# Kernel tuning notes

Hardware: AMD Instinct MI355X
Metric: run time of the kernel (lower is better)

## Reference

```python
import jax, jax.numpy as jnp
import numpy as np

B, N, DIM, HEADS, DIM_HEAD = 2, 2048, 1024, 16, 64
INNER = HEADS * DIM_HEAD  # 1024
SCALE = DIM_HEAD ** -0.5
EPS = 1e-5  # fp32 path in the source


def _layernorm_seq(x, g):
    # Faithful to the repo's LayerNorm: statistics over dim=1 (sequence axis),
    # unbiased=False variance, clamp(min=eps).rsqrt(), scale by g over last axis.
    mean = jnp.mean(x, axis=1, keepdims=True)            # [b,1,d]
    var = jnp.mean((x - mean) ** 2, axis=1, keepdims=True)
    return (x - mean) * jax.lax.rsqrt(jnp.maximum(var, EPS)) * g


def setup_inputs() -> dict:
    key = jax.random.key(0)
    ks = jax.random.split(key, 5)
    x = jax.random.normal(ks[0], (B, N, DIM), dtype=jnp.float32)
    rel_pos_bias = jax.random.normal(ks[1], (1, HEADS, N, N), dtype=jnp.float32)
    g = jnp.ones((DIM,), dtype=jnp.float32)
    wq = jax.random.normal(ks[2], (INNER, DIM), dtype=jnp.float32) * (DIM ** -0.5)
    wkv = jax.random.normal(ks[3], (2 * INNER, DIM), dtype=jnp.float32) * (DIM ** -0.5)
    wout = jax.random.normal(ks[4], (DIM, INNER), dtype=jnp.float32) * (INNER ** -0.5)
    return {"x": x, "rel_pos_bias": rel_pos_bias, "g": g, "wq": wq, "wkv": wkv, "wout": wout}


def reference(x, rel_pos_bias, g, wq, wkv, wout):
    # self-attention path: context = x, framerate = None
    xn = _layernorm_seq(x, g)           # [b,n,d]
    cn = xn                              # context is None -> same tensor, same norm
    q = jnp.einsum('bnd,ed->bne', xn, wq)        # [b,n,inner]
    kv = jnp.einsum('bnd,ed->bne', cn, wkv)      # [b,n,2*inner]
    k, v = jnp.split(kv, 2, axis=-1)
    def heads(t):
        return t.reshape(B, N, HEADS, DIM_HEAD).transpose(0, 2, 1, 3)  # b h n d
    q, k, v = heads(q) * SCALE, heads(k), heads(v)
    sim = jnp.einsum('bhid,bhjd->bhij', q, k) + rel_pos_bias
    attn = jax.nn.softmax(sim, axis=-1)
    out = jnp.einsum('bhij,bhjd->bhid', attn, v)
    out = out.transpose(0, 2, 1, 3).reshape(B, N, INNER)  # b n (h d)
    return jnp.einsum('bne,de->bnd', out, wout)
```

## Files before the change

kernel.cpp:

```cpp
#include <hip/hip_runtime.h>
#include <hip/hip_bf16.h>
#include <stdint.h>

#define B_ 2
#define N_ 2048
#define DIM_ 1024
#define HEADS_ 16
#define DH_ 64
#define EPS_ 1e-5f

typedef __attribute__((ext_vector_type(4))) float f32x4;
typedef __attribute__((ext_vector_type(8))) __bf16 bf16x8;
typedef __attribute__((ext_vector_type(4))) unsigned int u32x4;

__device__ __forceinline__ f32x4 mfma16(bf16x8 a, bf16x8 b, f32x4 c) {
  return __builtin_amdgcn_mfma_f32_16x16x32_bf16(a, b, c, 0, 0, 0);
}

__device__ __forceinline__ unsigned short f2bf(float x) {
  unsigned int u = __builtin_bit_cast(unsigned int, x);
  u += 0x7fffu + ((u >> 16) & 1u);
  return (unsigned short)(u >> 16);
}

__device__ __forceinline__ unsigned int cvt_pk_bf16(float lo, float hi) {
  unsigned int r;
  asm("v_cvt_pk_bf16_f32 %0, %1, %2" : "=v"(r) : "v"(lo), "v"(hi));
  return r;
}

__device__ __forceinline__ bf16x8 ld_frag(const unsigned short* p) {
  u32x4 v = *reinterpret_cast<const u32x4*>(p);
  return __builtin_bit_cast(bf16x8, v);
}

__device__ __forceinline__ void gload_lds16(const unsigned short* g, unsigned short* l) {
  __builtin_amdgcn_global_load_lds((const __attribute__((address_space(1))) void*)g,
                                   (__attribute__((address_space(3))) void*)l, 16, 0, 0);
}

__global__ __launch_bounds__(256) void ln_part(const float* __restrict__ x,
                                               float* __restrict__ ps,
                                               float* __restrict__ pss) {
  const int d = blockIdx.x * 256 + threadIdx.x;
  const int b = blockIdx.y >> 4, sp = blockIdx.y & 15;
  const float* xp = x + (size_t)(b * N_ + sp * 128) * DIM_ + d;
  float s = 0.f, ss = 0.f;
  for (int i = 0; i < 128; ++i) {
    float v = xp[(size_t)i * DIM_];
    s += v;
    ss += v * v;
  }
  int c = b * DIM_ + d;
  ps[sp * (B_ * DIM_) + c] = s;
  pss[sp * (B_ * DIM_) + c] = ss;
}

__global__ void ln_fin(const float* __restrict__ ps, const float* __restrict__ pss,
                       const float* __restrict__ g, float* __restrict__ meanA,
                       float* __restrict__ sclA) {
  int c = blockIdx.x * 256 + threadIdx.x;
  float s = 0.f, ss = 0.f;
#pragma unroll
  for (int sp = 0; sp < 16; ++sp) {
    s += ps[sp * (B_ * DIM_) + c];
    ss += pss[sp * (B_ * DIM_) + c];
  }
  float m = s * (1.f / N_);
  float v = ss * (1.f / N_) - m * m;
  meanA[c] = m;
  sclA[c] = rsqrtf(fmaxf(v, EPS_)) * g[c & (DIM_ - 1)];
}

__global__ __launch_bounds__(256) void ln_apply(const float* __restrict__ x,
                                                const float* __restrict__ meanA,
                                                const float* __restrict__ sclA,
                                                unsigned short* __restrict__ xn) {
  size_t t = (size_t)blockIdx.x * 256 + threadIdx.x;
  size_t base = t * 8;
  int d0 = (int)(base & (DIM_ - 1));
  int b = base >= (size_t)N_ * DIM_;
  int c = b * DIM_ + d0;
  const float4* xp = reinterpret_cast<const float4*>(x + base);
  const float4* mp = reinterpret_cast<const float4*>(meanA + c);
  const float4* sp = reinterpret_cast<const float4*>(sclA + c);
  float4 x0 = xp[0], x1 = xp[1];
  float4 m0 = mp[0], m1 = mp[1];
  float4 s0 = sp[0], s1 = sp[1];
  union {
    unsigned short u[8];
    u32x4 v;
  } o;
  o.u[0] = f2bf((x0.x - m0.x) * s0.x);
  o.u[1] = f2bf((x0.y - m0.y) * s0.y);
  o.u[2] = f2bf((x0.z - m0.z) * s0.z);
  o.u[3] = f2bf((x0.w - m0.w) * s0.w);
  o.u[4] = f2bf((x1.x - m1.x) * s1.x);
  o.u[5] = f2bf((x1.y - m1.y) * s1.y);
  o.u[6] = f2bf((x1.z - m1.z) * s1.z);
  o.u[7] = f2bf((x1.w - m1.w) * s1.w);
  *reinterpret_cast<u32x4*>(xn + base) = o.v;
}

__global__ __launch_bounds__(256) void cast_bf16(const float* __restrict__ src,
                                                 unsigned short* __restrict__ dst, float scale) {
  size_t t = (size_t)blockIdx.x * 256 + threadIdx.x;
  size_t base = t * 8;
  const float4* sp = reinterpret_cast<const float4*>(src + base);
  float4 a = sp[0], b4 = sp[1];
  union {
    unsigned short u[8];
    u32x4 v;
  } o;
  o.u[0] = f2bf(a.x * scale);
  o.u[1] = f2bf(a.y * scale);
  o.u[2] = f2bf(a.z * scale);
  o.u[3] = f2bf(a.w * scale);
  o.u[4] = f2bf(b4.x * scale);
  o.u[5] = f2bf(b4.y * scale);
  o.u[6] = f2bf(b4.z * scale);
  o.u[7] = f2bf(b4.w * scale);
  *reinterpret_cast<u32x4*>(dst + base) = o.v;
}

template <bool OUT_F32>
__global__ __launch_bounds__(256) void gemm_bt(const unsigned short* __restrict__ A,
                                               const unsigned short* __restrict__ W,
                                               void* __restrict__ Cout, int K, int ldc) {
  __shared__ unsigned short sA[128 * 64];
  __shared__ unsigned short sB[128 * 64];
  const int tid = threadIdx.x, lane = tid & 63, w = tid >> 6;
  const int wm = w >> 1, wn = w & 1;
  const int l15 = lane & 15, l4 = lane >> 4;
  const int m0 = blockIdx.y * 128, n0 = blockIdx.x * 128;
  f32x4 acc[4][4] = {};
  for (int kt = 0; kt < K; kt += 64) {
    __syncthreads();
#pragma unroll
    for (int p = 0; p < 4; ++p) {
      int flat = p * 256 + tid;
      int row = flat >> 3, c = flat & 7;
      int cs = c ^ (row & 7);
      gload_lds16(A + (size_t)(m0 + row) * K + kt + cs * 8, sA + (size_t)(p * 256 + w * 64) * 8);
      gload_lds16(W + (size_t)(n0 + row) * K + kt + cs * 8, sB + (size_t)(p * 256 + w * 64) * 8);
    }
    __syncthreads();
#pragma unroll
    for (int kk = 0; kk < 2; ++kk) {
      bf16x8 af[4], bfr[4];
#pragma unroll
      for (int i = 0; i < 4; ++i) {
        int rowA = wm * 64 + i * 16 + l15;
        af[i] = ld_frag(sA + rowA * 64 + (((kk * 4 + l4) ^ (rowA & 7)) * 8));
        int rowB = wn * 64 + i * 16 + l15;
        bfr[i] = ld_frag(sB + rowB * 64 + (((kk * 4 + l4) ^ (rowB & 7)) * 8));
      }
#pragma unroll
      for (int i = 0; i < 4; ++i)
#pragma unroll
        for (int j = 0; j < 4; ++j) acc[i][j] = mfma16(af[i], bfr[j], acc[i][j]);
    }
  }
#pragma unroll
  for (int i = 0; i < 4; ++i)
#pragma unroll
    for (int j = 0; j < 4; ++j)
#pragma unroll
      for (int r = 0; r < 4; ++r) {
        size_t off =
            (size_t)(m0 + wm * 64 + i * 16 + l4 * 4 + r) * ldc + (n0 + wn * 64 + j * 16 + l15);
        if (OUT_F32)
          ((float*)Cout)[off] = acc[i][j][r];
        else
          ((unsigned short*)Cout)[off] = f2bf(acc[i][j][r]);
      }
}

__global__ __launch_bounds__(256) void transpose_v(const unsigned short* __restrict__ qkv,
                                                   unsigned short* __restrict__ Vt) {
  __shared__ unsigned short tt[64][65];
  const int tid = threadIdx.x;
  const int h = blockIdx.y >> 1, b = blockIdx.y & 1;
  const int n0 = blockIdx.x * 64;
  const unsigned short* src = qkv + (size_t)(b * N_ + n0) * 3072 + 2048 + h * 64;
#pragma unroll
  for (int i = 0; i < 16; ++i) {
    int idx = i * 256 + tid;
    int r = idx >> 6, c = idx & 63;
    tt[r][c] = src[(size_t)r * 3072 + c];
  }
  __syncthreads();
  unsigned short* dst = Vt + (size_t)(b * HEADS_ + h) * 64 * N_ + n0;
#pragma unroll
  for (int i = 0; i < 16; ++i) {
    int idx = i * 256 + tid;
    int dh = idx >> 6, nn = idx & 63;
    dst[(size_t)dh * N_ + nn] = tt[nn][dh];
  }
}

__global__ __launch_bounds__(512, 4) void flash_attn(const unsigned short* __restrict__ qkv,
                                                     const float* __restrict__ bias,
                                                     const unsigned short* __restrict__ Vt,
                                                     unsigned short* __restrict__ Oatt) {
  __shared__ unsigned short sK[2][64 * 64];
  __shared__ unsigned short sV[2][64 * 64];
  __shared__ unsigned short sP[8 * 16 * 64];

  const int tid = threadIdx.x, lane = tid & 63, w = tid >> 6;
  const int l15 = lane & 15, l4 = lane >> 4;
  const int r = blockIdx.x;
  const int bh = r & 31, iblk = r >> 5;
  const int h = bh & 15, b = bh >> 4;
  const int i0 = iblk * 128;

  const unsigned short* Kg = qkv + (size_t)b * N_ * 3072 + 1024 + h * 64;
  const unsigned short* VtB = Vt + (size_t)(b * HEADS_ + h) * 64 * N_;
  const float* bias_q =
      bias + (size_t)h * N_ * N_ + (size_t)(i0 + w * 16 + l15) * N_ + l4 * 4;

  const int srow = tid >> 3, sc = tid & 7;
  const int scs = sc ^ (srow & 7);
  const size_t kSrcOff = (size_t)srow * 3072 + (size_t)scs * 8;
  const size_t vSrcOff = (size_t)srow * N_ + (size_t)scs * 8;
  unsigned short* kDst0 = sK[0] + (size_t)w * 512;
  unsigned short* kDst1 = sK[1] + (size_t)w * 512;
  unsigned short* vDst0 = sV[0] + (size_t)w * 512;
  unsigned short* vDst1 = sV[1] + (size_t)w * 512;

  bf16x8 qf[2];
  {
    const unsigned short* Qg =
        qkv + (size_t)(b * N_ + i0 + w * 16 + l15) * 3072 + h * 64 + l4 * 8;
    qf[0] = ld_frag(Qg);
    qf[1] = ld_frag(Qg + 32);
  }

  f32x4 o_t[4] = {};
  f32x4 stA[4], stB[4];
  float m_run = -1e30f, l_run = 0.f;
  const int sw = l15 & 7;

  unsigned int* sPu = reinterpret_cast<unsigned int*>(sP + (size_t)w * 16 * 64);
  const unsigned short* sPw = sP + (size_t)w * 16 * 64;

  gload_lds16(Kg + kSrcOff, kDst0);
  gload_lds16(VtB + vSrcOff, vDst0);
  stA[0] = *reinterpret_cast<const f32x4*>(bias_q);
  stA[1] = *reinterpret_cast<const f32x4*>(bias_q + 16);
  stA[2] = *reinterpret_cast<const f32x4*>(bias_q + 32);
  stA[3] = *reinterpret_cast<const f32x4*>(bias_q + 48);
  __syncthreads();

  const int NT = N_ / 64;

#define TILE_BODY(T, SKC, SVC, KDN, VDN, SC, SN)                               \
  {                                                                            \
    if ((T) + 1 < NT) {                                                        \
      const size_t jn = (size_t)((T) + 1) * 64;                                \
      gload_lds16(Kg + jn * 3072 + kSrcOff, KDN);                              \
      gload_lds16(VtB + jn + vSrcOff, VDN);                                    \
      __builtin_amdgcn_sched_barrier(0);  \
      SN[0] = *reinterpret_cast<const f32x4*>(bias_q + jn);                    \
      SN[1] = *reinterpret_cast<const f32x4*>(bias_q + jn + 16);               \
      SN[2] = *reinterpret_cast<const f32x4*>(bias_q + jn + 32);               \
      SN[3] = *reinterpret_cast<const f32x4*>(bias_q + jn + 48);               \
    }                                                                          \
                 \
    __builtin_amdgcn_s_setprio(1);                                             \
    _Pragma("unroll") for (int kj = 0; kj < 4; ++kj) {                         \
      int row = kj * 16 + l15;                                                 \
      bf16x8 kf0 = ld_frag(SKC + row * 64 + ((l4 ^ sw) * 8));                  \
      bf16x8 kf1 = ld_frag(SKC + row * 64 + (((4 + l4) ^ sw) * 8));            \
      SC[kj] = mfma16(kf0, qf[0], SC[kj]);                                     \
      SC[kj] = mfma16(kf1, qf[1], SC[kj]);                                     \
    }                                                                          \
    __builtin_amdgcn_s_setprio(0);                                             \
                  \
    float mx = fmaxf(fmaxf(fmaxf(SC[0][0], SC[0][1]), fmaxf(SC[0][2], SC[0][3])), \
                     fmaxf(fmaxf(SC[1][0], SC[1][1]), fmaxf(SC[1][2], SC[1][3]))); \
    mx = fmaxf(mx, fmaxf(fmaxf(fmaxf(SC[2][0], SC[2][1]), fmaxf(SC[2][2], SC[2][3])), \
                         fmaxf(fmaxf(SC[3][0], SC[3][1]), fmaxf(SC[3][2], SC[3][3])))); \
    mx = fmaxf(mx, __shfl_xor(mx, 16));                                        \
    mx = fmaxf(mx, __shfl_xor(mx, 32));                                        \
    float mn = fmaxf(m_run, mx);                                               \
    float alpha = __expf(m_run - mn);                                          \
    float rs = 0.f;                                                            \
    _Pragma("unroll") for (int kj = 0; kj < 4; ++kj) {                         \
      _Pragma("unroll") for (int rr = 0; rr < 4; ++rr) {                       \
        float p = __expf(SC[kj][rr] - mn);                                     \
        SC[kj][rr] = p;                                                        \
        rs += p;                                                               \
      }                                                                        \
    }                                                                          \
    rs += __shfl_xor(rs, 16);                                                  \
    rs += __shfl_xor(rs, 32);                                                  \
    l_run = l_run * alpha + rs;                                                \
    m_run = mn;                                                                \
    _Pragma("unroll") for (int dj = 0; dj < 4; ++dj) {                         \
      o_t[dj][0] *= alpha;                                                     \
      o_t[dj][1] *= alpha;                                                     \
      o_t[dj][2] *= alpha;                                                     \
      o_t[dj][3] *= alpha;                                                     \
    }                                                                          \
         \
    _Pragma("unroll") for (int kj = 0; kj < 4; ++kj) {                         \
      unsigned int v0 = cvt_pk_bf16(SC[kj][0], SC[kj][1]);                     \
      unsigned int v1 = cvt_pk_bf16(SC[kj][2], SC[kj][3]);                     \
      int cc = (kj * 2 + (l4 >> 1)) ^ sw;                                      \
      uint2 pv;                                                                \
      pv.x = v0;                                                               \
      pv.y = v1;                                                               \
      *reinterpret_cast<uint2*>(sPu + l15 * 32 + cc * 4 + (l4 & 1) * 2) = pv;  \
    }                                                                          \
                                                           \
    bf16x8 pb0 = ld_frag(sPw + l15 * 64 + ((l4 ^ sw) * 8));                    \
    bf16x8 pb1 = ld_frag(sPw + l15 * 64 + (((4 + l4) ^ sw) * 8));              \
    __builtin_amdgcn_s_setprio(1);                                             \
    _Pragma("unroll") for (int dj = 0; dj < 4; ++dj) {                         \
      int row = dj * 16 + l15;                                                 \
      bf16x8 vf0 = ld_frag(SVC + row * 64 + ((l4 ^ sw) * 8));                  \
      bf16x8 vf1 = ld_frag(SVC + row * 64 + (((4 + l4) ^ sw) * 8));            \
      o_t[dj] = mfma16(vf0, pb0, o_t[dj]);                                     \
      o_t[dj] = mfma16(vf1, pb1, o_t[dj]);                                     \
    }                                                                          \
    __builtin_amdgcn_s_setprio(0);                                             \
    if ((T) != NT - 1) {                                                       \
          \
                    \
      asm volatile("s_waitcnt vmcnt(4)" ::: "memory");                         \
      __builtin_amdgcn_s_barrier();                                            \
    }                                                                          \
  }

  const unsigned short* sK0c = sK[0];
  const unsigned short* sK1c = sK[1];
  const unsigned short* sV0c = sV[0];
  const unsigned short* sV1c = sV[1];
  for (int t = 0; t < NT; t += 2) {
    TILE_BODY(t, sK0c, sV0c, kDst1, vDst1, stA, stB)
    TILE_BODY(t + 1, sK1c, sV1c, kDst0, vDst0, stB, stA)
  }
#undef TILE_BODY

  float inv = 1.f / l_run;
  unsigned short* orow =
      Oatt + (size_t)(b * N_ + i0 + w * 16 + l15) * 1024 + h * 64 + l4 * 4;
#pragma unroll
  for (int dj = 0; dj < 4; ++dj) {
    union {
      unsigned short u[4];
      unsigned long long v;
    } pk;
    pk.u[0] = f2bf(o_t[dj][0] * inv);
    pk.u[1] = f2bf(o_t[dj][1] * inv);
    pk.u[2] = f2bf(o_t[dj][2] * inv);
    pk.u[3] = f2bf(o_t[dj][3] * inv);
    *reinterpret_cast<unsigned long long*>(orow + dj * 16) = pk.v;
  }
}

extern "C" void kernel_launch(void* const* d_in, const int* in_sizes, int n_in, void* d_out,
                              int out_size, void* d_ws, size_t ws_size, hipStream_t stream) {
  const float* x = (const float*)d_in[0];
  const float* bias = (const float*)d_in[1];
  const float* g = (const float*)d_in[2];
  const float* wq = (const float*)d_in[3];
  const float* wkv = (const float*)d_in[4];
  const float* wout = (const float*)d_in[5];
  float* out = (float*)d_out;

  float* ps = (float*)d_ws;
  float* pss = ps + 16 * B_ * DIM_;
  float* meanA = pss + 16 * B_ * DIM_;
  float* sclA = meanA + B_ * DIM_;
  unsigned short* xn = (unsigned short*)(sclA + B_ * DIM_);
  unsigned short* Wqkv = xn + (size_t)4096 * 1024;
  unsigned short* WoutB = Wqkv + (size_t)3072 * 1024;
  unsigned short* qkvb = WoutB + (size_t)1024 * 1024;
  unsigned short* Vt = qkvb + (size_t)4096 * 3072;
  unsigned short* Oatt = xn;

  ln_part<<<dim3(DIM_ / 256, B_ * 16), 256, 0, stream>>>(x, ps, pss);
  ln_fin<<<dim3((B_ * DIM_) / 256), 256, 0, stream>>>(ps, pss, g, meanA, sclA);
  ln_apply<<<dim3((B_ * N_ * DIM_) / 2048), 256, 0, stream>>>(x, meanA, sclA, xn);
  cast_bf16<<<dim3((DIM_ * DIM_) / 2048), 256, 0, stream>>>(wq, Wqkv, 0.125f);
  cast_bf16<<<dim3((2 * DIM_ * DIM_) / 2048), 256, 0, stream>>>(wkv, Wqkv + (size_t)DIM_ * DIM_,
                                                                1.0f);
  cast_bf16<<<dim3((DIM_ * DIM_) / 2048), 256, 0, stream>>>(wout, WoutB, 1.0f);
  gemm_bt<false><<<dim3(3072 / 128, 4096 / 128), 256, 0, stream>>>(xn, Wqkv, qkvb, DIM_, 3072);
  transpose_v<<<dim3(N_ / 64, B_ * HEADS_), 256, 0, stream>>>(qkvb, Vt);
  flash_attn<<<dim3(512), 512, 0, stream>>>(qkvb, bias, Vt, Oatt);
  gemm_bt<true><<<dim3(1024 / 128, 4096 / 128), 256, 0, stream>>>(Oatt, WoutB, out, DIM_, 1024);
}
```

Before: 190.2 us.

## Give each attention wave 32 query rows to reuse K/V fragments across two tiles

The flash attention kernel now runs 4 waves of 256 threads per block instead of 8. Each wave handles two 16-row query fragments and reuses every K and V fragment it loads from LDS for both. Staging is split into four async loads per thread, the vmcnt wait is raised to match, and softmax state is duplicated per fragment. This halves LDS fragment reads per MFMA but doubles accumulator and bias registers per thread, which lowers occupancy and leaves fewer waves to hide the latency of the fp32 bias loads.

```diff
diff --git a/kernel.cpp b/kernel.cpp
--- a/kernel.cpp
+++ b/kernel.cpp
@@ -199,13 +199,13 @@
   }
 }
 
-__global__ __launch_bounds__(512, 4) void flash_attn(const unsigned short* __restrict__ qkv,
+__global__ __launch_bounds__(256, 2) void flash_attn(const unsigned short* __restrict__ qkv,
                                                      const float* __restrict__ bias,
                                                      const unsigned short* __restrict__ Vt,
                                                      unsigned short* __restrict__ Oatt) {
   __shared__ unsigned short sK[2][64 * 64];
   __shared__ unsigned short sV[2][64 * 64];
-  __shared__ unsigned short sP[8 * 16 * 64];
+  __shared__ unsigned short sP[4 * 32 * 64];
 
   const int tid = threadIdx.x, lane = tid & 63, w = tid >> 6;
   const int l15 = lane & 15, l4 = lane >> 4;
@@ -213,150 +213,199 @@
   const int bh = r & 31, iblk = r >> 5;
   const int h = bh & 15, b = bh >> 4;
   const int i0 = iblk * 128;
+  const int qbase = i0 + w * 32;
 
   const unsigned short* Kg = qkv + (size_t)b * N_ * 3072 + 1024 + h * 64;
   const unsigned short* VtB = Vt + (size_t)(b * HEADS_ + h) * 64 * N_;
-  const float* bias_q =
-      bias + (size_t)h * N_ * N_ + (size_t)(i0 + w * 16 + l15) * N_ + l4 * 4;
-
-  const int srow = tid >> 3, sc = tid & 7;
-  const int scs = sc ^ (srow & 7);
-  const size_t kSrcOff = (size_t)srow * 3072 + (size_t)scs * 8;
-  const size_t vSrcOff = (size_t)srow * N_ + (size_t)scs * 8;
-  unsigned short* kDst0 = sK[0] + (size_t)w * 512;
-  unsigned short* kDst1 = sK[1] + (size_t)w * 512;
-  unsigned short* vDst0 = sV[0] + (size_t)w * 512;
-  unsigned short* vDst1 = sV[1] + (size_t)w * 512;
-
-  bf16x8 qf[2];
+  const float* bias_q0 =
+      bias + (size_t)h * N_ * N_ + (size_t)(qbase + l15) * N_ + l4 * 4;
+  const float* bias_q1 = bias_q0 + 16 * N_;
+
+  const int row0 = tid >> 3, c0 = tid & 7;
+  const int cs0 = c0 ^ (row0 & 7);
+  const unsigned short* KgS = Kg + (size_t)row0 * 3072 + cs0 * 8;
+  const unsigned short* VtS = VtB + (size_t)row0 * N_ + cs0 * 8;
+
+#define STAGE(BUF, JN)                                                     \
+  gload_lds16(KgS + (size_t)(JN) * 3072, sK[BUF] + w * 512);               \
+  gload_lds16(KgS + (size_t)(JN) * 3072 + 32 * 3072, sK[BUF] + 2048 + w * 512); \
+  gload_lds16(VtS + (JN), sV[BUF] + w * 512);                              \
+  gload_lds16(VtS + (JN) + 32 * (size_t)N_, sV[BUF] + 2048 + w * 512);
+
+  bf16x8 qf00, qf01, qf10, qf11;
   {
-    const unsigned short* Qg =
-        qkv + (size_t)(b * N_ + i0 + w * 16 + l15) * 3072 + h * 64 + l4 * 8;
-    qf[0] = ld_frag(Qg);
-    qf[1] = ld_frag(Qg + 32);
-  }
-
-  f32x4 o_t[4] = {};
-  f32x4 stA[4], stB[4];
-  float m_run = -1e30f, l_run = 0.f;
+    const unsigned short* Qg0 =
+        qkv + (size_t)(b * N_ + qbase + l15) * 3072 + h * 64 + l4 * 8;
+    const unsigned short* Qg1 = Qg0 + (size_t)16 * 3072;
+    qf00 = ld_frag(Qg0);
+    qf01 = ld_frag(Qg0 + 32);
+    qf10 = ld_frag(Qg1);
+    qf11 = ld_frag(Qg1 + 32);
+  }
+
+  f32x4 o_t[8] = {};
+  f32x4 stA[8], stB[8];
+  float m0_run = -1e30f, l0_run = 0.f;
+  float m1_run = -1e30f, l1_run = 0.f;
   const int sw = l15 & 7;
 
-  unsigned int* sPu = reinterpret_cast<unsigned int*>(sP + (size_t)w * 16 * 64);
-  const unsigned short* sPw = sP + (size_t)w * 16 * 64;
-
-  gload_lds16(Kg + kSrcOff, kDst0);
-  gload_lds16(VtB + vSrcOff, vDst0);
-  stA[0] = *reinterpret_cast<const f32x4*>(bias_q);
-  stA[1] = *reinterpret_cast<const f32x4*>(bias_q + 16);
-  stA[2] = *reinterpret_cast<const f32x4*>(bias_q + 32);
-  stA[3] = *reinterpret_cast<const f32x4*>(bias_q + 48);
+  unsigned int* sPu = reinterpret_cast<unsigned int*>(sP + (size_t)w * 2048);
+  const unsigned short* sPw = sP + (size_t)w * 2048;
+
+  STAGE(0, 0)
+#pragma unroll
+  for (int kj = 0; kj < 4; ++kj) {
+    stA[kj] = *reinterpret_cast<const f32x4*>(bias_q0 + kj * 16);
+    stA[4 + kj] = *reinterpret_cast<const f32x4*>(bias_q1 + kj * 16);
+  }
   __syncthreads();
 
   const int NT = N_ / 64;
 
-#define TILE_BODY(T, SKC, SVC, KDN, VDN, SC, SN)                               \
+#define TILE_BODY(T, CUR, NXT, SC, SN)                                         \
   {                                                                            \
     if ((T) + 1 < NT) {                                                        \
       const size_t jn = (size_t)((T) + 1) * 64;                                \
-      gload_lds16(Kg + jn * 3072 + kSrcOff, KDN);                              \
-      gload_lds16(VtB + jn + vSrcOff, VDN);                                    \
+      STAGE(NXT, jn)                                                           \
       __builtin_amdgcn_sched_barrier(0);  \
-      SN[0] = *reinterpret_cast<const f32x4*>(bias_q + jn);                    \
-      SN[1] = *reinterpret_cast<const f32x4*>(bias_q + jn + 16);               \
-      SN[2] = *reinterpret_cast<const f32x4*>(bias_q + jn + 32);               \
-      SN[3] = *reinterpret_cast<const f32x4*>(bias_q + jn + 48);               \
-    }                                                                          \
-                 \
+      _Pragma("unroll") for (int kj = 0; kj < 4; ++kj) {                       \
+        SN[kj] = *reinterpret_cast<const f32x4*>(bias_q0 + jn + kj * 16);      \
+        SN[4 + kj] = *reinterpret_cast<const f32x4*>(bias_q1 + jn + kj * 16);  \
+      }                                                                        \
+    }                                                                          \
+    const unsigned short* sKc = sK[CUR];                                       \
+    const unsigned short* sVc = sV[CUR];                                       \
+                  \
     __builtin_amdgcn_s_setprio(1);                                             \
     _Pragma("unroll") for (int kj = 0; kj < 4; ++kj) {                         \
       int row = kj * 16 + l15;                                                 \
-      bf16x8 kf0 = ld_frag(SKC + row * 64 + ((l4 ^ sw) * 8));                  \
-      bf16x8 kf1 = ld_frag(SKC + row * 64 + (((4 + l4) ^ sw) * 8));            \
-      SC[kj] = mfma16(kf0, qf[0], SC[kj]);                                     \
-      SC[kj] = mfma16(kf1, qf[1], SC[kj]);                                     \
+      bf16x8 kf0 = ld_frag(sKc + row * 64 + ((l4 ^ sw) * 8));                  \
+      bf16x8 kf1 = ld_frag(sKc + row * 64 + (((4 + l4) ^ sw) * 8));            \
+      SC[kj] = mfma16(kf0, qf00, SC[kj]);                                      \
+      SC[kj] = mfma16(kf1, qf01, SC[kj]);                                      \
+      SC[4 + kj] = mfma16(kf0, qf10, SC[4 + kj]);                              \
+      SC[4 + kj] = mfma16(kf1, qf11, SC[4 + kj]);                              \
     }                                                                          \
     __builtin_amdgcn_s_setprio(0);                                             \
-                  \
-    float mx = fmaxf(fmaxf(fmaxf(SC[0][0], SC[0][1]), fmaxf(SC[0][2], SC[0][3])), \
-                     fmaxf(fmaxf(SC[1][0], SC[1][1]), fmaxf(SC[1][2], SC[1][3]))); \
-    mx = fmaxf(mx, fmaxf(fmaxf(fmaxf(SC[2][0], SC[2][1]), fmaxf(SC[2][2], SC[2][3])), \
-                         fmaxf(fmaxf(SC[3][0], SC[3][1]), fmaxf(SC[3][2], SC[3][3])))); \
-    mx = fmaxf(mx, __shfl_xor(mx, 16));                                        \
-    mx = fmaxf(mx, __shfl_xor(mx, 32));                                        \
-    float mn = fmaxf(m_run, mx);                                               \
-    float alpha = __expf(m_run - mn);                                          \
-    float rs = 0.f;                                                            \
-    _Pragma("unroll") for (int kj = 0; kj < 4; ++kj) {                         \
-      _Pragma("unroll") for (int rr = 0; rr < 4; ++rr) {                       \
-        float p = __expf(SC[kj][rr] - mn);                                     \
-        SC[kj][rr] = p;                                                        \
-        rs += p;                                                               \
-      }                                                                        \
-    }                                                                          \
-    rs += __shfl_xor(rs, 16);                                                  \
-    rs += __shfl_xor(rs, 32);                                                  \
-    l_run = l_run * alpha + rs;                                                \
-    m_run = mn;                                                                \
-    _Pragma("unroll") for (int dj = 0; dj < 4; ++dj) {                         \
-      o_t[dj][0] *= alpha;                                                     \
-      o_t[dj][1] *= alpha;                                                     \
-      o_t[dj][2] *= alpha;                                                     \
-      o_t[dj][3] *= alpha;                                                     \
-    }                                                                          \
-         \
-    _Pragma("unroll") for (int kj = 0; kj < 4; ++kj) {                         \
-      unsigned int v0 = cvt_pk_bf16(SC[kj][0], SC[kj][1]);                     \
-      unsigned int v1 = cvt_pk_bf16(SC[kj][2], SC[kj][3]);                     \
-      int cc = (kj * 2 + (l4 >> 1)) ^ sw;                                      \
-      uint2 pv;                                                                \
-      pv.x = v0;                                                               \
-      pv.y = v1;                                                               \
-      *reinterpret_cast<uint2*>(sPu + l15 * 32 + cc * 4 + (l4 & 1) * 2) = pv;  \
-    }                                                                          \
-                                                           \
-    bf16x8 pb0 = ld_frag(sPw + l15 * 64 + ((l4 ^ sw) * 8));                    \
-    bf16x8 pb1 = ld_frag(sPw + l15 * 64 + (((4 + l4) ^ sw) * 8));              \
+                               \
+    {                                                                          \
+      float mx = fmaxf(fmaxf(fmaxf(SC[0][0], SC[0][1]), fmaxf(SC[0][2], SC[0][3])), \
+                       fmaxf(fmaxf(SC[1][0], SC[1][1]), fmaxf(SC[1][2], SC[1][3]))); \
+      mx = fmaxf(mx, fmaxf(fmaxf(fmaxf(SC[2][0], SC[2][1]), fmaxf(SC[2][2], SC[2][3])), \
+                           fmaxf(fmaxf(SC[3][0], SC[3][1]), fmaxf(SC[3][2], SC[3][3])))); \
+      mx = fmaxf(mx, __shfl_xor(mx, 16));                                      \
+      mx = fmaxf(mx, __shfl_xor(mx, 32));                                      \
+      float mn = fmaxf(m0_run, mx);                                            \
+      float alpha = __expf(m0_run - mn);                                       \
+      float rs = 0.f;                                                          \
+      _Pragma("unroll") for (int kj = 0; kj < 4; ++kj) {                       \
+        _Pragma("unroll") for (int rr = 0; rr < 4; ++rr) {                     \
+          float p = __expf(SC[kj][rr] - mn);                                   \
+          SC[kj][rr] = p;                                                      \
+          rs += p;                                                             \
+        }                                                                      \
+      }                                                                        \
+      rs += __shfl_xor(rs, 16);                                                \
+      rs += __shfl_xor(rs, 32);                                                \
+      l0_run = l0_run * alpha + rs;                                            \
+      m0_run = mn;                                                             \
+      _Pragma("unroll") for (int dj = 0; dj < 4; ++dj) {                       \
+        o_t[dj][0] *= alpha;                                                   \
+        o_t[dj][1] *= alpha;                                                   \
+        o_t[dj][2] *= alpha;                                                   \
+        o_t[dj][3] *= alpha;                                                   \
+      }                                                                        \
+    }                                                                          \
+                          \
+    {                                                                          \
+      float mx = fmaxf(fmaxf(fmaxf(SC[4][0], SC[4][1]), fmaxf(SC[4][2], SC[4][3])), \
+                       fmaxf(fmaxf(SC[5][0], SC[5][1]), fmaxf(SC[5][2], SC[5][3]))); \
+      mx = fmaxf(mx, fmaxf(fmaxf(fmaxf(SC[6][0], SC[6][1]), fmaxf(SC[6][2], SC[6][3])), \
+                           fmaxf(fmaxf(SC[7][0], SC[7][1]), fmaxf(SC[7][2], SC[7][3])))); \
+      mx = fmaxf(mx, __shfl_xor(mx, 16));                                      \
+      mx = fmaxf(mx, __shfl_xor(mx, 32));                                      \
+      float mn = fmaxf(m1_run, mx);                                            \
+      float alpha = __expf(m1_run - mn);                                       \
+      float rs = 0.f;                                                          \
+      _Pragma("unroll") for (int kj = 0; kj < 4; ++kj) {                       \
+        _Pragma("unroll") for (int rr = 0; rr < 4; ++rr) {                     \
+          float p = __expf(SC[4 + kj][rr] - mn);                               \
+          SC[4 + kj][rr] = p;                                                  \
+          rs += p;                                                             \
+        }                                                                      \
+      }                                                                        \
+      rs += __shfl_xor(rs, 16);                                                \
+      rs += __shfl_xor(rs, 32);                                                \
+      l1_run = l1_run * alpha + rs;                                            \
+      m1_run = mn;                                                             \
+      _Pragma("unroll") for (int dj = 0; dj < 4; ++dj) {                       \
+        o_t[4 + dj][0] *= alpha;                                               \
+        o_t[4 + dj][1] *= alpha;                                               \
+        o_t[4 + dj][2] *= alpha;                                               \
+        o_t[4 + dj][3] *= alpha;                                               \
+      }                                                                        \
+    }                                                                          \
+                   \
+    _Pragma("unroll") for (int f = 0; f < 2; ++f) {                            \
+      _Pragma("unroll") for (int kj = 0; kj < 4; ++kj) {                       \
+        unsigned int v0 = cvt_pk_bf16(SC[f * 4 + kj][0], SC[f * 4 + kj][1]);   \
+        unsigned int v1 = cvt_pk_bf16(SC[f * 4 + kj][2], SC[f * 4 + kj][3]);   \
+        int cc = (kj * 2 + (l4 >> 1)) ^ sw;                                    \
+        uint2 pv;                                                              \
+        pv.x = v0;                                                             \
+        pv.y = v1;                                                             \
+        *reinterpret_cast<uint2*>(sPu + (f * 16 + l15) * 32 + cc * 4 +         \
+                                  (l4 & 1) * 2) = pv;                          \
+      }                                                                        \
+    }                                                                          \
+                                 \
+    bf16x8 pb00 = ld_frag(sPw + l15 * 64 + ((l4 ^ sw) * 8));                   \
+    bf16x8 pb01 = ld_frag(sPw + l15 * 64 + (((4 + l4) ^ sw) * 8));             \
+    bf16x8 pb10 = ld_frag(sPw + (16 + l15) * 64 + ((l4 ^ sw) * 8));            \
+    bf16x8 pb11 = ld_frag(sPw + (16 + l15) * 64 + (((4 + l4) ^ sw) * 8));      \
     __builtin_amdgcn_s_setprio(1);                                             \
     _Pragma("unroll") for (int dj = 0; dj < 4; ++dj) {                         \
       int row = dj * 16 + l15;                                                 \
-      bf16x8 vf0 = ld_frag(SVC + row * 64 + ((l4 ^ sw) * 8));                  \
-      bf16x8 vf1 = ld_frag(SVC + row * 64 + (((4 + l4) ^ sw) * 8));            \
-      o_t[dj] = mfma16(vf0, pb0, o_t[dj]);                                     \
-      o_t[dj] = mfma16(vf1, pb1, o_t[dj]);                                     \
+      bf16x8 vf0 = ld_frag(sVc + row * 64 + ((l4 ^ sw) * 8));                  \
+      bf16x8 vf1 = ld_frag(sVc + row * 64 + (((4 + l4) ^ sw) * 8));            \
+      o_t[dj] = mfma16(vf0, pb00, o_t[dj]);                                    \
+      o_t[dj] = mfma16(vf1, pb01, o_t[dj]);                                    \
+      o_t[4 + dj] = mfma16(vf0, pb10, o_t[4 + dj]);                            \
+      o_t[4 + dj] = mfma16(vf1, pb11, o_t[4 + dj]);                            \
     }                                                                          \
     __builtin_amdgcn_s_setprio(0);                                             \
     if ((T) != NT - 1) {                                                       \
           \
                     \
-      asm volatile("s_waitcnt vmcnt(4)" ::: "memory");                         \
+      asm volatile("s_waitcnt vmcnt(8)" ::: "memory");                         \
       __builtin_amdgcn_s_barrier();                                            \
     }                                                                          \
   }
 
-  const unsigned short* sK0c = sK[0];
-  const unsigned short* sK1c = sK[1];
-  const unsigned short* sV0c = sV[0];
-  const unsigned short* sV1c = sV[1];
   for (int t = 0; t < NT; t += 2) {
-    TILE_BODY(t, sK0c, sV0c, kDst1, vDst1, stA, stB)
-    TILE_BODY(t + 1, sK1c, sV1c, kDst0, vDst0, stB, stA)
+    TILE_BODY(t, 0, 1, stA, stB)
+    TILE_BODY(t + 1, 1, 0, stB, stA)
   }
 #undef TILE_BODY
-
-  float inv = 1.f / l_run;
-  unsigned short* orow =
-      Oatt + (size_t)(b * N_ + i0 + w * 16 + l15) * 1024 + h * 64 + l4 * 4;
-#pragma unroll
-  for (int dj = 0; dj < 4; ++dj) {
-    union {
-      unsigned short u[4];
-      unsigned long long v;
-    } pk;
-    pk.u[0] = f2bf(o_t[dj][0] * inv);
-    pk.u[1] = f2bf(o_t[dj][1] * inv);
-    pk.u[2] = f2bf(o_t[dj][2] * inv);
-    pk.u[3] = f2bf(o_t[dj][3] * inv);
-    *reinterpret_cast<unsigned long long*>(orow + dj * 16) = pk.v;
+#undef STAGE
+
+#pragma unroll
+  for (int f = 0; f < 2; ++f) {
+    float inv = 1.f / (f ? l1_run : l0_run);
+    unsigned short* orow =
+        Oatt + (size_t)(b * N_ + qbase + f * 16 + l15) * 1024 + h * 64 + l4 * 4;
+#pragma unroll
+    for (int dj = 0; dj < 4; ++dj) {
+      union {
+        unsigned short u[4];
+        unsigned long long v;
+      } pk;
+      pk.u[0] = f2bf(o_t[f * 4 + dj][0] * inv);
+      pk.u[1] = f2bf(o_t[f * 4 + dj][1] * inv);
+      pk.u[2] = f2bf(o_t[f * 4 + dj][2] * inv);
+      pk.u[3] = f2bf(o_t[f * 4 + dj][3] * inv);
+      *reinterpret_cast<unsigned long long*>(orow + dj * 16) = pk.v;
+    }
   }
 }
 
@@ -390,6 +439,6 @@
   cast_bf16<<<dim3((DIM_ * DIM_) / 2048), 256, 0, stream>>>(wout, WoutB, 1.0f);
   gemm_bt<false><<<dim3(3072 / 128, 4096 / 128), 256, 0, stream>>>(xn, Wqkv, qkvb, DIM_, 3072);
   transpose_v<<<dim3(N_ / 64, B_ * HEADS_), 256, 0, stream>>>(qkvb, Vt);
-  flash_attn<<<dim3(512), 512, 0, stream>>>(qkvb, bias, Vt, Oatt);
+  flash_attn<<<dim3(512), 256, 0, stream>>>(qkvb, bias, Vt, Oatt);
   gemm_bt<true><<<dim3(1024 / 128, 4096 / 128), 256, 0, stream>>>(Oatt, WoutB, out, DIM_, 1024);
 }
```

Measured after the change: 191.9 us. About the same (+0.9%).

## Switch flash attention to 32x32 MFMA with in-register P via permlane swaps

Applied to the files above, without the earlier changes.

Rewrites the attention kernel so each wave handles 32 query rows with 32x32x16 bf16 MFMAs instead of 16x16x32. The softmax probabilities are rearranged into the B-operand layout with permlane32_swap, which removes the LDS round trip through sP. Row reductions also use permlane swaps. Blocks shrink to 4 waves (256 threads) and each thread issues more staging loads. The larger tile raises register pressure and reduces the number of waves per block.

```diff
diff --git a/kernel.cpp b/kernel.cpp
--- a/kernel.cpp
+++ b/kernel.cpp
@@ -10,11 +10,18 @@
 #define EPS_ 1e-5f
 
 typedef __attribute__((ext_vector_type(4))) float f32x4;
+typedef __attribute__((ext_vector_type(8))) float f32x8;
+typedef __attribute__((ext_vector_type(16))) float f32x16;
 typedef __attribute__((ext_vector_type(8))) __bf16 bf16x8;
 typedef __attribute__((ext_vector_type(4))) unsigned int u32x4;
+typedef __attribute__((ext_vector_type(2))) unsigned int u32x2;
 
 __device__ __forceinline__ f32x4 mfma16(bf16x8 a, bf16x8 b, f32x4 c) {
   return __builtin_amdgcn_mfma_f32_16x16x32_bf16(a, b, c, 0, 0, 0);
+}
+
+__device__ __forceinline__ f32x16 mfma32(bf16x8 a, bf16x8 b, f32x16 c) {
+  return __builtin_amdgcn_mfma_f32_32x32x16_bf16(a, b, c, 0, 0, 0);
 }
 
 __device__ __forceinline__ unsigned short f2bf(float x) {
@@ -28,6 +35,9 @@
   asm("v_cvt_pk_bf16_f32 %0, %1, %2" : "=v"(r) : "v"(lo), "v"(hi));
   return r;
 }
+
+__device__ __forceinline__ float uasf(unsigned int u) { return __builtin_bit_cast(float, u); }
+__device__ __forceinline__ unsigned int fasu(float f) { return __builtin_bit_cast(unsigned int, f); }
 
 __device__ __forceinline__ bf16x8 ld_frag(const unsigned short* p) {
   u32x4 v = *reinterpret_cast<const u32x4*>(p);
@@ -199,164 +209,205 @@
   }
 }
 
-__global__ __launch_bounds__(512, 4) void flash_attn(const unsigned short* __restrict__ qkv,
+__global__ __launch_bounds__(256, 2) void flash_attn(const unsigned short* __restrict__ qkv,
                                                      const float* __restrict__ bias,
                                                      const unsigned short* __restrict__ Vt,
                                                      unsigned short* __restrict__ Oatt) {
   __shared__ unsigned short sK[2][64 * 64];
   __shared__ unsigned short sV[2][64 * 64];
-  __shared__ unsigned short sP[8 * 16 * 64];
 
   const int tid = threadIdx.x, lane = tid & 63, w = tid >> 6;
-  const int l15 = lane & 15, l4 = lane >> 4;
+  const int l31 = lane & 31, hi = lane >> 5;
   const int r = blockIdx.x;
   const int bh = r & 31, iblk = r >> 5;
   const int h = bh & 15, b = bh >> 4;
   const int i0 = iblk * 128;
+  const int qbase = i0 + w * 32;
 
   const unsigned short* Kg = qkv + (size_t)b * N_ * 3072 + 1024 + h * 64;
   const unsigned short* VtB = Vt + (size_t)(b * HEADS_ + h) * 64 * N_;
-  const float* bias_q =
-      bias + (size_t)h * N_ * N_ + (size_t)(i0 + w * 16 + l15) * N_ + l4 * 4;
-
-  const int srow = tid >> 3, sc = tid & 7;
-  const int scs = sc ^ (srow & 7);
-  const size_t kSrcOff = (size_t)srow * 3072 + (size_t)scs * 8;
-  const size_t vSrcOff = (size_t)srow * N_ + (size_t)scs * 8;
-  unsigned short* kDst0 = sK[0] + (size_t)w * 512;
-  unsigned short* kDst1 = sK[1] + (size_t)w * 512;
-  unsigned short* vDst0 = sV[0] + (size_t)w * 512;
-  unsigned short* vDst1 = sV[1] + (size_t)w * 512;
-
-  bf16x8 qf[2];
+  const float* bias_l =
+      bias + (size_t)h * N_ * N_ + (size_t)(qbase + l31) * N_ + 4 * hi;
+
+  const int row0 = tid >> 3, c0 = tid & 7;
+  const int cs0 = c0 ^ (row0 & 7);
+  const unsigned short* KgS = Kg + (size_t)row0 * 3072 + cs0 * 8;
+  const unsigned short* VtS = VtB + (size_t)row0 * N_ + cs0 * 8;
+
+#define STAGE(BUF, JN)                                                          \
+  gload_lds16(KgS + (size_t)(JN) * 3072, sK[BUF] + w * 512);                    \
+  gload_lds16(KgS + (size_t)(JN) * 3072 + 32 * 3072, sK[BUF] + 2048 + w * 512); \
+  gload_lds16(VtS + (JN), sV[BUF] + w * 512);                                   \
+  gload_lds16(VtS + (JN) + 32 * (size_t)N_, sV[BUF] + 2048 + w * 512);
+
+  bf16x8 qf0, qf1, qf2, qf3;
   {
     const unsigned short* Qg =
-        qkv + (size_t)(b * N_ + i0 + w * 16 + l15) * 3072 + h * 64 + l4 * 8;
-    qf[0] = ld_frag(Qg);
-    qf[1] = ld_frag(Qg + 32);
-  }
-
-  f32x4 o_t[4] = {};
-  f32x4 stA[4], stB[4];
+        qkv + (size_t)(b * N_ + qbase + l31) * 3072 + h * 64 + hi * 8;
+    qf0 = ld_frag(Qg);
+    qf1 = ld_frag(Qg + 16);
+    qf2 = ld_frag(Qg + 32);
+    qf3 = ld_frag(Qg + 48);
+  }
+
+  f32x16 o0 = {}, o1 = {};
+  f32x16 sA0, sA1, sB0, sB1;
   float m_run = -1e30f, l_run = 0.f;
-  const int sw = l15 & 7;
-
-  unsigned int* sPu = reinterpret_cast<unsigned int*>(sP + (size_t)w * 16 * 64);
-  const unsigned short* sPw = sP + (size_t)w * 16 * 64;
-
-  gload_lds16(Kg + kSrcOff, kDst0);
-  gload_lds16(VtB + vSrcOff, vDst0);
-  stA[0] = *reinterpret_cast<const f32x4*>(bias_q);
-  stA[1] = *reinterpret_cast<const f32x4*>(bias_q + 16);
-  stA[2] = *reinterpret_cast<const f32x4*>(bias_q + 32);
-  stA[3] = *reinterpret_cast<const f32x4*>(bias_q + 48);
+
+#define LDBIAS(DST, OFF)                                                   \
+  {                                                                        \
+    f32x4 t0 = *reinterpret_cast<const f32x4*>(bias_l + (OFF));            \
+    f32x4 t1 = *reinterpret_cast<const f32x4*>(bias_l + (OFF) + 8);        \
+    f32x4 t2 = *reinterpret_cast<const f32x4*>(bias_l + (OFF) + 16);       \
+    f32x4 t3 = *reinterpret_cast<const f32x4*>(bias_l + (OFF) + 24);       \
+    f32x8 u0_ = __builtin_shufflevector(t0, t1, 0, 1, 2, 3, 4, 5, 6, 7);   \
+    f32x8 u1_ = __builtin_shufflevector(t2, t3, 0, 1, 2, 3, 4, 5, 6, 7);   \
+    DST = __builtin_shufflevector(u0_, u1_, 0, 1, 2, 3, 4, 5, 6, 7, 8, 9,  \
+                                  10, 11, 12, 13, 14, 15);                 \
+  }
+
+#define FRAG(OUT, SRC, RB, CH)                                          \
+  {                                                                     \
+    int row_ = (RB) + l31;                                              \
+    OUT = ld_frag((SRC) + row_ * 64 + (((CH) ^ (row_ & 7)) * 8));       \
+  }
+
+  STAGE(0, 0)
+  LDBIAS(sA0, 0)
+  LDBIAS(sA1, 32)
   __syncthreads();
 
   const int NT = N_ / 64;
 
-#define TILE_BODY(T, SKC, SVC, KDN, VDN, SC, SN)                               \
+#define TILE_BODY(T, CUR, NXT, S0, S1, S0N, S1N)                               \
   {                                                                            \
     if ((T) + 1 < NT) {                                                        \
       const size_t jn = (size_t)((T) + 1) * 64;                                \
-      gload_lds16(Kg + jn * 3072 + kSrcOff, KDN);                              \
-      gload_lds16(VtB + jn + vSrcOff, VDN);                                    \
+      STAGE(NXT, jn)                                                           \
       __builtin_amdgcn_sched_barrier(0);  \
-      SN[0] = *reinterpret_cast<const f32x4*>(bias_q + jn);                    \
-      SN[1] = *reinterpret_cast<const f32x4*>(bias_q + jn + 16);               \
-      SN[2] = *reinterpret_cast<const f32x4*>(bias_q + jn + 32);               \
-      SN[3] = *reinterpret_cast<const f32x4*>(bias_q + jn + 48);               \
-    }                                                                          \
+      LDBIAS(S0N, jn)                                                          \
+      LDBIAS(S1N, jn + 32)                                                     \
+    }                                                                          \
+    const unsigned short* sKc = sK[CUR];                                       \
+    const unsigned short* sVc = sV[CUR];                                       \
                  \
     __builtin_amdgcn_s_setprio(1);                                             \
-    _Pragma("unroll") for (int kj = 0; kj < 4; ++kj) {                         \
-      int row = kj * 16 + l15;                                                 \
-      bf16x8 kf0 = ld_frag(SKC + row * 64 + ((l4 ^ sw) * 8));                  \
-      bf16x8 kf1 = ld_frag(SKC + row * 64 + (((4 + l4) ^ sw) * 8));            \
-      SC[kj] = mfma16(kf0, qf[0], SC[kj]);                                     \
-      SC[kj] = mfma16(kf1, qf[1], SC[kj]);                                     \
+    {                                                                          \
+      bf16x8 kf;                                                               \
+      FRAG(kf, sKc, 0, 0 + hi) S0 = mfma32(kf, qf0, S0);                       \
+      FRAG(kf, sKc, 0, 2 + hi) S0 = mfma32(kf, qf1, S0);                       \
+      FRAG(kf, sKc, 0, 4 + hi) S0 = mfma32(kf, qf2, S0);                       \
+      FRAG(kf, sKc, 0, 6 + hi) S0 = mfma32(kf, qf3, S0);                       \
+      FRAG(kf, sKc, 32, 0 + hi) S1 = mfma32(kf, qf0, S1);                      \
+      FRAG(kf, sKc, 32, 2 + hi) S1 = mfma32(kf, qf1, S1);                      \
+      FRAG(kf, sKc, 32, 4 + hi) S1 = mfma32(kf, qf2, S1);                      \
+      FRAG(kf, sKc, 32, 6 + hi) S1 = mfma32(kf, qf3, S1);                      \
     }                                                                          \
     __builtin_amdgcn_s_setprio(0);                                             \
-                  \
-    float mx = fmaxf(fmaxf(fmaxf(SC[0][0], SC[0][1]), fmaxf(SC[0][2], SC[0][3])), \
-                     fmaxf(fmaxf(SC[1][0], SC[1][1]), fmaxf(SC[1][2], SC[1][3]))); \
-    mx = fmaxf(mx, fmaxf(fmaxf(fmaxf(SC[2][0], SC[2][1]), fmaxf(SC[2][2], SC[2][3])), \
-                         fmaxf(fmaxf(SC[3][0], SC[3][1]), fmaxf(SC[3][2], SC[3][3])))); \
-    mx = fmaxf(mx, __shfl_xor(mx, 16));                                        \
-    mx = fmaxf(mx, __shfl_xor(mx, 32));                                        \
+        \
+    float mx = S0[0];                                                          \
+    _Pragma("unroll") for (int i = 1; i < 16; ++i) mx = fmaxf(mx, S0[i]);      \
+    _Pragma("unroll") for (int i = 0; i < 16; ++i) mx = fmaxf(mx, S1[i]);      \
+    {                                                                          \
+      auto pr_ = __builtin_amdgcn_permlane32_swap(fasu(mx), fasu(mx), false,   \
+                                                  false);                      \
+      mx = fmaxf(uasf(pr_[0]), uasf(pr_[1]));                                  \
+    }                                                                          \
     float mn = fmaxf(m_run, mx);                                               \
     float alpha = __expf(m_run - mn);                                          \
+    _Pragma("unroll") for (int i = 0; i < 16; ++i) S0[i] = __expf(S0[i] - mn); \
+    _Pragma("unroll") for (int i = 0; i < 16; ++i) S1[i] = __expf(S1[i] - mn); \
     float rs = 0.f;                                                            \
-    _Pragma("unroll") for (int kj = 0; kj < 4; ++kj) {                         \
-      _Pragma("unroll") for (int rr = 0; rr < 4; ++rr) {                       \
-        float p = __expf(SC[kj][rr] - mn);                                     \
-        SC[kj][rr] = p;                                                        \
-        rs += p;                                                               \
-      }                                                                        \
-    }                                                                          \
-    rs += __shfl_xor(rs, 16);                                                  \
-    rs += __shfl_xor(rs, 32);                                                  \
+    _Pragma("unroll") for (int i = 0; i < 16; ++i) rs += S0[i];                \
+    _Pragma("unroll") for (int i = 0; i < 16; ++i) rs += S1[i];                \
+    {                                                                          \
+      auto pr_ = __builtin_amdgcn_permlane32_swap(fasu(rs), fasu(rs), false,   \
+                                                  false);                      \
+      rs = uasf(pr_[0]) + uasf(pr_[1]);                                        \
+    }                                                                          \
     l_run = l_run * alpha + rs;                                                \
     m_run = mn;                                                                \
-    _Pragma("unroll") for (int dj = 0; dj < 4; ++dj) {                         \
-      o_t[dj][0] *= alpha;                                                     \
-      o_t[dj][1] *= alpha;                                                     \
-      o_t[dj][2] *= alpha;                                                     \
-      o_t[dj][3] *= alpha;                                                     \
-    }                                                                          \
-         \
-    _Pragma("unroll") for (int kj = 0; kj < 4; ++kj) {                         \
-      unsigned int v0 = cvt_pk_bf16(SC[kj][0], SC[kj][1]);                     \
-      unsigned int v1 = cvt_pk_bf16(SC[kj][2], SC[kj][3]);                     \
-      int cc = (kj * 2 + (l4 >> 1)) ^ sw;                                      \
-      uint2 pv;                                                                \
-      pv.x = v0;                                                               \
-      pv.y = v1;                                                               \
-      *reinterpret_cast<uint2*>(sPu + l15 * 32 + cc * 4 + (l4 & 1) * 2) = pv;  \
-    }                                                                          \
-                                                           \
-    bf16x8 pb0 = ld_frag(sPw + l15 * 64 + ((l4 ^ sw) * 8));                    \
-    bf16x8 pb1 = ld_frag(sPw + l15 * 64 + (((4 + l4) ^ sw) * 8));              \
+    _Pragma("unroll") for (int i = 0; i < 16; ++i) o0[i] *= alpha;             \
+    _Pragma("unroll") for (int i = 0; i < 16; ++i) o1[i] *= alpha;             \
+      \
+      \
+    bf16x8 pb0, pb1, pb2, pb3;                                                 \
+    {                                                                          \
+      unsigned int w0 = cvt_pk_bf16(S0[0], S0[1]), w1 = cvt_pk_bf16(S0[2], S0[3]);   \
+      unsigned int w2 = cvt_pk_bf16(S0[4], S0[5]), w3 = cvt_pk_bf16(S0[6], S0[7]);   \
+      unsigned int w4 = cvt_pk_bf16(S0[8], S0[9]), w5 = cvt_pk_bf16(S0[10], S0[11]); \
+      unsigned int w6 = cvt_pk_bf16(S0[12], S0[13]),                           \
+                   w7 = cvt_pk_bf16(S0[14], S0[15]);                           \
+      auto rA = __builtin_amdgcn_permlane32_swap(w0, w2, false, false);        \
+      auto rB = __builtin_amdgcn_permlane32_swap(w1, w3, false, false);        \
+      auto rC = __builtin_amdgcn_permlane32_swap(w4, w6, false, false);        \
+      auto rD = __builtin_amdgcn_permlane32_swap(w5, w7, false, false);        \
+      u32x4 pw;                                                                \
+      pw[0] = rA[0]; pw[1] = rB[0]; pw[2] = rA[1]; pw[3] = rB[1];              \
+      pb0 = __builtin_bit_cast(bf16x8, pw);                                    \
+      pw[0] = rC[0]; pw[1] = rD[0]; pw[2] = rC[1]; pw[3] = rD[1];              \
+      pb1 = __builtin_bit_cast(bf16x8, pw);                                    \
+    }                                                                          \
+    {                                                                          \
+      unsigned int w0 = cvt_pk_bf16(S1[0], S1[1]), w1 = cvt_pk_bf16(S1[2], S1[3]);   \
+      unsigned int w2 = cvt_pk_bf16(S1[4], S1[5]), w3 = cvt_pk_bf16(S1[6], S1[7]);   \
+      unsigned int w4 = cvt_pk_bf16(S1[8], S1[9]), w5 = cvt_pk_bf16(S1[10], S1[11]); \
+      unsigned int w6 = cvt_pk_bf16(S1[12], S1[13]),                           \
+                   w7 = cvt_pk_bf16(S1[14], S1[15]);                           \
+      auto rA = __builtin_amdgcn_permlane32_swap(w0, w2, false, false);        \
+      auto rB = __builtin_amdgcn_permlane32_swap(w1, w3, false, false);        \
+      auto rC = __builtin_amdgcn_permlane32_swap(w4, w6, false, false);        \
+      auto rD = __builtin_amdgcn_permlane32_swap(w5, w7, false, false);        \
+      u32x4 pw;                                                                \
+      pw[0] = rA[0]; pw[1] = rB[0]; pw[2] = rA[1]; pw[3] = rB[1];              \
+      pb2 = __builtin_bit_cast(bf16x8, pw);                                    \
+      pw[0] = rC[0]; pw[1] = rD[0]; pw[2] = rC[1]; pw[3] = rD[1];              \
+      pb3 = __builtin_bit_cast(bf16x8, pw);                                    \
+    }                                                                          \
+                                  \
     __builtin_amdgcn_s_setprio(1);                                             \
-    _Pragma("unroll") for (int dj = 0; dj < 4; ++dj) {                         \
-      int row = dj * 16 + l15;                                                 \
-      bf16x8 vf0 = ld_frag(SVC + row * 64 + ((l4 ^ sw) * 8));                  \
-      bf16x8 vf1 = ld_frag(SVC + row * 64 + (((4 + l4) ^ sw) * 8));            \
-      o_t[dj] = mfma16(vf0, pb0, o_t[dj]);                                     \
-      o_t[dj] = mfma16(vf1, pb1, o_t[dj]);                                     \
+    {                                                                          \
+      bf16x8 vf;                                                               \
+      FRAG(vf, sVc, 0, 0 + hi) o0 = mfma32(vf, pb0, o0);                       \
+      FRAG(vf, sVc, 0, 2 + hi) o0 = mfma32(vf, pb1, o0);                       \
+      FRAG(vf, sVc, 0, 4 + hi) o0 = mfma32(vf, pb2, o0);                       \
+      FRAG(vf, sVc, 0, 6 + hi) o0 = mfma32(vf, pb3, o0);                       \
+      FRAG(vf, sVc, 32, 0 + hi) o1 = mfma32(vf, pb0, o1);                      \
+      FRAG(vf, sVc, 32, 2 + hi) o1 = mfma32(vf, pb1, o1);                      \
+      FRAG(vf, sVc, 32, 4 + hi) o1 = mfma32(vf, pb2, o1);                      \
+      FRAG(vf, sVc, 32, 6 + hi) o1 = mfma32(vf, pb3, o1);                      \
     }                                                                          \
     __builtin_amdgcn_s_setprio(0);                                             \
     if ((T) != NT - 1) {                                                       \
           \
                     \
-      asm volatile("s_waitcnt vmcnt(4)" ::: "memory");                         \
+      asm volatile("s_waitcnt vmcnt(8)" ::: "memory");                         \
       __builtin_amdgcn_s_barrier();                                            \
     }                                                                          \
   }
 
-  const unsigned short* sK0c = sK[0];
-  const unsigned short* sK1c = sK[1];
-  const unsigned short* sV0c = sV[0];
-  const unsigned short* sV1c = sV[1];
   for (int t = 0; t < NT; t += 2) {
-    TILE_BODY(t, sK0c, sV0c, kDst1, vDst1, stA, stB)
-    TILE_BODY(t + 1, sK1c, sV1c, kDst0, vDst0, stB, stA)
+    TILE_BODY(t, 0, 1, sA0, sA1, sB0, sB1)
+    TILE_BODY(t + 1, 1, 0, sB0, sB1, sA0, sA1)
   }
 #undef TILE_BODY
+#undef STAGE
+#undef LDBIAS
+#undef FRAG
 
   float inv = 1.f / l_run;
   unsigned short* orow =
-      Oatt + (size_t)(b * N_ + i0 + w * 16 + l15) * 1024 + h * 64 + l4 * 4;
-#pragma unroll
-  for (int dj = 0; dj < 4; ++dj) {
-    union {
-      unsigned short u[4];
-      unsigned long long v;
-    } pk;
-    pk.u[0] = f2bf(o_t[dj][0] * inv);
-    pk.u[1] = f2bf(o_t[dj][1] * inv);
-    pk.u[2] = f2bf(o_t[dj][2] * inv);
-    pk.u[3] = f2bf(o_t[dj][3] * inv);
-    *reinterpret_cast<unsigned long long*>(orow + dj * 16) = pk.v;
+      Oatt + (size_t)(b * N_ + qbase + l31) * 1024 + h * 64 + hi * 4;
+#pragma unroll
+  for (int g = 0; g < 4; ++g) {
+    u32x2 pk0;
+    pk0[0] = cvt_pk_bf16(o0[g * 4 + 0] * inv, o0[g * 4 + 1] * inv);
+    pk0[1] = cvt_pk_bf16(o0[g * 4 + 2] * inv, o0[g * 4 + 3] * inv);
+    *reinterpret_cast<u32x2*>(orow + g * 8) = pk0;
+    u32x2 pk1;
+    pk1[0] = cvt_pk_bf16(o1[g * 4 + 0] * inv, o1[g * 4 + 1] * inv);
+    pk1[1] = cvt_pk_bf16(o1[g * 4 + 2] * inv, o1[g * 4 + 3] * inv);
+    *reinterpret_cast<u32x2*>(orow + 32 + g * 8) = pk1;
   }
 }
 
@@ -390,6 +441,6 @@
   cast_bf16<<<dim3((DIM_ * DIM_) / 2048), 256, 0, stream>>>(wout, WoutB, 1.0f);
   gemm_bt<false><<<dim3(3072 / 128, 4096 / 128), 256, 0, stream>>>(xn, Wqkv, qkvb, DIM_, 3072);
   transpose_v<<<dim3(N_ / 64, B_ * HEADS_), 256, 0, stream>>>(qkvb, Vt);
-  flash_attn<<<dim3(512), 512, 0, stream>>>(qkvb, bias, Vt, Oatt);
+  flash_attn<<<dim3(512), 256, 0, stream>>>(qkvb, bias, Vt, Oatt);
   gemm_bt<true><<<dim3(1024 / 128, 4096 / 128), 256, 0, stream>>>(Oatt, WoutB, out, DIM_, 1024);
 }
```

Result: slower. 203.1 us (+6.8%).
